# Kernel tuning notes

Hardware: AMD Instinct MI355X
Metric: run time of the kernel (lower is better)

## Reference

```python
import jax, jax.numpy as jnp
import numpy as np

EMBED_DIM = 1024
NUM_HEADS = 16
HEAD_DIM = EMBED_DIM // NUM_HEADS
B, S = 2, 2048


def setup_inputs() -> dict:
    key = jax.random.key(0)
    ks = jax.random.split(key, 9)
    d = EMBED_DIM
    scale = 1.0 / np.sqrt(d)
    inp = {
        "x": jax.random.normal(ks[0], (B, S, d), dtype=jnp.float32),
        "mask": jnp.ones((B, S), dtype=jnp.int32),
        "Wq": jax.random.normal(ks[1], (d, d), dtype=jnp.float32) * scale,
        "bq": jnp.zeros((d,), dtype=jnp.float32),
        "Wk": jax.random.normal(ks[2], (d, d), dtype=jnp.float32) * scale,
        "bk": jnp.zeros((d,), dtype=jnp.float32),
        "Wv": jax.random.normal(ks[3], (d, d), dtype=jnp.float32) * scale,
        "bv": jnp.zeros((d,), dtype=jnp.float32),
        "Wo": jax.random.normal(ks[4], (d, d), dtype=jnp.float32) * scale,
        "bo": jnp.zeros((d,), dtype=jnp.float32),
    }
    return inp


def reference(x, mask, Wq, bq, Wk, bk, Wv, bv, Wo, bo):
    b, s, _ = x.shape
    # projections; torch Linear computes x @ W.T + b
    q = (x @ Wq.T + bq).reshape(b, s, NUM_HEADS, HEAD_DIM).transpose(0, 2, 1, 3)
    k = (x @ Wk.T + bk).reshape(b, s, NUM_HEADS, HEAD_DIM).transpose(0, 2, 1, 3)
    v = (x @ Wv.T + bv).reshape(b, s, NUM_HEADS, HEAD_DIM).transpose(0, 2, 1, 3)
    scores = jnp.einsum("bhqd,bhkd->bhqk", q, k) / np.sqrt(HEAD_DIM)  # (B,H,S,S)
    m = (mask == 0)[:, None, None, :]  # broadcast over heads and query pos
    scores = jnp.where(m, jnp.float32(-1e9), scores)
    attn = jax.nn.softmax(scores, axis=-1)
    out = jnp.einsum("bhqk,bhkd->bhqd", attn, v)
    out = out.transpose(0, 2, 1, 3).reshape(b, s, EMBED_DIM)
    return out @ Wo.T + bo
```

## Files before the change

kernel.cpp:

```cpp
#include <hip/hip_runtime.h>

#define EMBED 1024
#define NHEAD 16
#define HDIM  64
#define BB    2
#define SS    2048

typedef __bf16 bf16x8 __attribute__((ext_vector_type(8)));
typedef float  f32x4  __attribute__((ext_vector_type(4)));
typedef _Float16 f16x4 __attribute__((ext_vector_type(4)));
typedef _Float16 f16x8 __attribute__((ext_vector_type(8)));
typedef __fp16 hf16x2 __attribute__((ext_vector_type(2)));

#if defined(__has_builtin)
#if __has_builtin(__builtin_amdgcn_exp2f)
#define EXP2(x) __builtin_amdgcn_exp2f(x)
#else
#define EXP2(x) exp2f(x)
#endif
#else
#define EXP2(x) exp2f(x)
#endif

__device__ __forceinline__ unsigned short f2bf(float f) {
  union { float f; unsigned u; } v; v.f = f;
  unsigned r = v.u + 0x7fffu + ((v.u >> 16) & 1u);
  return (unsigned short)(r >> 16);
}

__device__ __forceinline__ float bf2f(unsigned short u) {
  union { unsigned u; float f; } v; v.u = ((unsigned)u) << 16;
  return v.f;
}

__device__ __forceinline__ unsigned short f2h(float f) {
  union { _Float16 h; unsigned short u; } t;
  t.h = (_Float16)f;
  return t.u;
}

__device__ __forceinline__ void g2l16(const unsigned short* g, unsigned short* l) {
  __builtin_amdgcn_global_load_lds(
      (const __attribute__((address_space(1))) unsigned int*)g,
      (__attribute__((address_space(3))) unsigned int*)l, 16, 0, 0);
}

__global__ __launch_bounds__(256)
void cvt5_kernel(const float* __restrict__ x,  const float* __restrict__ Wq,
                 const float* __restrict__ Wk, const float* __restrict__ Wv,
                 const float* __restrict__ Wo, const int* __restrict__ mask,
                 unsigned short* __restrict__ xb,  unsigned short* __restrict__ Wqb,
                 unsigned short* __restrict__ Wkb, unsigned short* __restrict__ Wvb,
                 unsigned short* __restrict__ Wob, float* __restrict__ mbias) {
  const int i = blockIdx.x * 256 + threadIdx.x;
  if (i < (1 << 21)) {
    const float* src;
    unsigned short* dst;
    int j;
    if (i < (1 << 20)) {
      src = x; dst = xb; j = i;
    } else {
      const int t = i - (1 << 20);
      const int r = t >> 18;
      j = t & ((1 << 18) - 1);
      src = (r == 0) ? Wq : (r == 1) ? Wk : (r == 2) ? Wv : Wo;
      dst = (r == 0) ? Wqb : (r == 1) ? Wkb : (r == 2) ? Wvb : Wob;
    }
    const float4 f = ((const float4*)src)[j];
    ushort4 u;
    u.x = f2bf(f.x); u.y = f2bf(f.y); u.z = f2bf(f.z); u.w = f2bf(f.w);
    ((ushort4*)dst)[j] = u;
  } else {
    const int j = i - (1 << 21);
    const int4 m = ((const int4*)mask)[j];
    float4 o;
    o.x = m.x ? 0.f : -1e30f; o.y = m.y ? 0.f : -1e30f;
    o.z = m.z ? 0.f : -1e30f; o.w = m.w ? 0.f : -1e30f;
    ((float4*)mbias)[j] = o;
  }
}

template <typename EpiFn>
__device__ __forceinline__
void gemm_core(const unsigned short* __restrict__ A,
               const unsigned short* __restrict__ Bm,
               int m0, int n0, EpiFn epi) {
  __shared__ unsigned short sA[128 * 64];
  __shared__ unsigned short sB[128 * 64];
  const int tid = threadIdx.x;
  const int l  = tid & 63;
  const int w  = tid >> 6;
  const int lm = l & 15;
  const int qd = l >> 4;
  const int wm = w & 1;
  const int wn = w >> 1;

  f32x4 acc[4][4];
#pragma unroll
  for (int i = 0; i < 4; ++i)
#pragma unroll
    for (int j = 0; j < 4; ++j) acc[i][j] = (f32x4){0.f, 0.f, 0.f, 0.f};

  for (int k0 = 0; k0 < EMBED; k0 += 64) {
#pragma unroll
    for (int i = 0; i < 4; ++i) {
      const int t = i * 256 + tid;
      const int r = t >> 3;
      const int c = (t & 7) ^ (r & 7);
      g2l16(A + (m0 + r) * EMBED + k0 + c * 8, &sA[(i * 256 + (w << 6)) * 8]);
      g2l16(Bm + (n0 + r) * EMBED + k0 + c * 8, &sB[(i * 256 + (w << 6)) * 8]);
    }
    __syncthreads();
#pragma unroll
    for (int kk = 0; kk < 2; ++kk) {
      bf16x8 af[4], bfr[4];
#pragma unroll
      for (int mi = 0; mi < 4; ++mi) {
        const int R = wm * 64 + mi * 16 + lm;
        const int ch = R * 8 + (((kk << 2) + qd) ^ (R & 7));
        af[mi] = *(const bf16x8*)&sA[ch * 8];
      }
#pragma unroll
      for (int ni = 0; ni < 4; ++ni) {
        const int R = wn * 64 + ni * 16 + lm;
        const int ch = R * 8 + (((kk << 2) + qd) ^ (R & 7));
        bfr[ni] = *(const bf16x8*)&sB[ch * 8];
      }
#pragma unroll
      for (int mi = 0; mi < 4; ++mi)
#pragma unroll
        for (int ni = 0; ni < 4; ++ni)
          acc[mi][ni] = __builtin_amdgcn_mfma_f32_16x16x32_bf16(
              af[mi], bfr[ni], acc[mi][ni], 0, 0, 0);
    }
    __syncthreads();
  }

#pragma unroll
  for (int mi = 0; mi < 4; ++mi)
#pragma unroll
    for (int ni = 0; ni < 4; ++ni) {
      const int mb = m0 + wm * 64 + mi * 16 + qd * 4;
      const int n  = n0 + wn * 64 + ni * 16 + lm;
      epi(acc[mi][ni], mb, n);
    }
}

__device__ __forceinline__ void decode_tile(int flat, int& a0, int& b0) {
  const int sub = flat & 15;
  const int g = flat >> 4;
  a0 = ((g >> 2) * 2 + (sub >> 3));
  b0 = ((g & 3) * 8 + (sub & 7));
}

__global__ __launch_bounds__(256)
void gemm_qkv(const unsigned short* __restrict__ xb,
              const unsigned short* __restrict__ Wqb,
              const unsigned short* __restrict__ Wkb,
              const unsigned short* __restrict__ Wvb,
              const float* __restrict__ bq, const float* __restrict__ bk,
              const float* __restrict__ bv,
              unsigned short* __restrict__ Qb, unsigned short* __restrict__ Kb,
              unsigned short* __restrict__ VTb) {
  const int z = blockIdx.y;
  int a0, b0;
  decode_tile(blockIdx.x, a0, b0);
  if (z < 2) {
    const unsigned short* A = z ? Wkb : Wqb;
    const float* bias = z ? bk : bq;
    unsigned short* O = z ? Kb : Qb;
    const float scale = z ? 1.0f : 0.125f * 1.4426950408889634f;
    gemm_core(A, xb, a0 * 128, b0 * 128, [&](const f32x4& v, int mb, int n) {
      const float4 bvv = *(const float4*)&bias[mb];
      const int h = mb >> 6, d0 = mb & 63;
      const int b = n >> 11, s = n & 2047;
      ushort4 u;
      u.x = f2bf((v.x + bvv.x) * scale); u.y = f2bf((v.y + bvv.y) * scale);
      u.z = f2bf((v.z + bvv.z) * scale); u.w = f2bf((v.w + bvv.w) * scale);
      *(ushort4*)&O[(((b * NHEAD + h) * SS) + s) * HDIM + d0] = u;
    });
  } else {
    gemm_core(xb, Wvb, b0 * 128, a0 * 128, [&](const f32x4& v, int mb, int n) {
      const float bvv = bv[n];
      const int b = mb >> 11, s = mb & 2047;
      const int h = n >> 6, d = n & 63;
      const int col = (s & ~31) + ((s >> 2) & 3) * 8 + ((s >> 4) & 1) * 4;
      ushort4 u;
      u.x = f2h(v.x + bvv); u.y = f2h(v.y + bvv);
      u.z = f2h(v.z + bvv); u.w = f2h(v.w + bvv);
      *(ushort4*)&VTb[(((b * NHEAD + h) * HDIM) + d) * SS + col] = u;
    });
  }
}

__global__ __launch_bounds__(256)
void gemm_out(const unsigned short* __restrict__ Wob,
              const unsigned short* __restrict__ Ob,
              const float* __restrict__ bo, float* __restrict__ out) {
  int a0, b0;
  decode_tile(blockIdx.x, a0, b0);
  gemm_core(Wob, Ob, a0 * 128, b0 * 128, [&](const f32x4& v, int mb, int n) {
    const float4 bvv = *(const float4*)&bo[mb];
    float4 o;
    o.x = v.x + bvv.x; o.y = v.y + bvv.y; o.z = v.z + bvv.z; o.w = v.w + bvv.w;
    *(float4*)&out[n * EMBED + mb] = o;
  });
}

__global__ __launch_bounds__(256)
void attn_kernel(const unsigned short* __restrict__ Q,
                 const unsigned short* __restrict__ K,
                 const unsigned short* __restrict__ VT,
                 const float* __restrict__ mbias,
                 unsigned short* __restrict__ Op0,
                 unsigned short* __restrict__ Op1,
                 float* __restrict__ Lpart) {
  __shared__ unsigned short sK[2][64 * 64];
  __shared__ unsigned short sV[2][64 * 64];
  __shared__ float sM[1024];
  const int tid = threadIdx.x;
  const int l = tid & 63, w = tid >> 6;
  const int lm = l & 15, qd = l >> 4;
  const int b = blockIdx.z & 1, sp = blockIdx.z >> 1, h = blockIdx.y;
  const int q0 = blockIdx.x * 128 + w * 32;
  const unsigned short* Qh = Q + ((b * NHEAD + h) * SS) * HDIM;
  const unsigned short* Kh = K + ((b * NHEAD + h) * SS) * HDIM;
  const unsigned short* Vh = VT + ((b * NHEAD + h) * HDIM) * SS;
  const int k0 = sp * (SS / 2);
  unsigned short* Op = sp ? Op1 : Op0;
  float* Lp = Lpart + sp * (BB * NHEAD * SS);

  *(float4*)&sM[tid * 4] = *(const float4*)&mbias[b * SS + k0 + tid * 4];

  bf16x8 qf[2][2];
#pragma unroll
  for (int g = 0; g < 2; ++g) {
    qf[g][0] = *(const bf16x8*)&Qh[(q0 + g * 16 + lm) * HDIM + qd * 8];
    qf[g][1] = *(const bf16x8*)&Qh[(q0 + g * 16 + lm) * HDIM + 32 + qd * 8];
  }

  f32x4 Od[2][4];
#pragma unroll
  for (int g = 0; g < 2; ++g)
#pragma unroll
    for (int i = 0; i < 4; ++i) Od[g][i] = (f32x4){0.f, 0.f, 0.f, 0.f};
  float lsum[2] = {0.f, 0.f};

  auto stage = [&](int kb, int buf) {
#pragma unroll
    for (int i = 0; i < 2; ++i) {
      const int t = i * 256 + tid;
      const int r = t >> 3;
      const int c = (t & 7) ^ (r & 7);
      g2l16(Kh + (kb + r) * HDIM + c * 8, &sK[buf][(i * 256 + (w << 6)) * 8]);
      g2l16(Vh + r * SS + kb + c * 8, &sV[buf][(i * 256 + (w << 6)) * 8]);
    }
  };

  const int nIt = (SS / 2) / 64;
  stage(k0, 0);
  for (int it = 0; it < nIt; ++it) {
    __syncthreads();
    if (it + 1 < nIt) stage(k0 + (it + 1) * 64, (it + 1) & 1);
    const unsigned short* bK = sK[it & 1];
    const unsigned short* bV = sV[it & 1];
    const int mof = it * 64;

    f16x4 pf[2][4];
#pragma unroll
    for (int j = 0; j < 4; ++j) {
      const int R = j * 16 + lm;
      const bf16x8 k0f = *(const bf16x8*)&bK[(R * 8 + (qd ^ (lm & 7))) * 8];
      const bf16x8 k1f = *(const bf16x8*)&bK[(R * 8 + ((4 + qd) ^ (lm & 7))) * 8];
      const f32x4 binit = *(const f32x4*)&sM[mof + j * 16 + qd * 4];
#pragma unroll
      for (int g = 0; g < 2; ++g) {
        f32x4 t0 = binit;
        t0 = __builtin_amdgcn_mfma_f32_16x16x32_bf16(k0f, qf[g][0], t0, 0, 0, 0);
        t0 = __builtin_amdgcn_mfma_f32_16x16x32_bf16(k1f, qf[g][1], t0, 0, 0, 0);
        const float p0 = EXP2(t0[0]);
        const float p1 = EXP2(t0[1]);
        const float p2 = EXP2(t0[2]);
        const float p3 = EXP2(t0[3]);
        lsum[g] += (p0 + p1) + (p2 + p3);
        union { hf16x2 v[2]; f16x4 f; } pk;
        pk.v[0] = __builtin_amdgcn_cvt_pkrtz(p0, p1);
        pk.v[1] = __builtin_amdgcn_cvt_pkrtz(p2, p3);
        pf[g][j] = pk.f;
      }
    }

#pragma unroll
    for (int dt = 0; dt < 4; ++dt) {
      const int row = dt * 16 + lm;
#pragma unroll
      for (int p = 0; p < 2; ++p) {
        const int ch = (p * 4 + qd) ^ (lm & 7);
        const f16x8 v8 = *(const f16x8*)&bV[row * 64 + ch * 8];
        const f16x4 vlo = __builtin_shufflevector(v8, v8, 0, 1, 2, 3);
        const f16x4 vhi = __builtin_shufflevector(v8, v8, 4, 5, 6, 7);
#pragma unroll
        for (int g = 0; g < 2; ++g) {
          Od[g][dt] = __builtin_amdgcn_mfma_f32_16x16x16f16(vlo, pf[g][2 * p],
                                                            Od[g][dt], 0, 0, 0);
          Od[g][dt] = __builtin_amdgcn_mfma_f32_16x16x16f16(vhi, pf[g][2 * p + 1],
                                                            Od[g][dt], 0, 0, 0);
        }
      }
    }
  }

#pragma unroll
  for (int g = 0; g < 2; ++g) {
    float ls = lsum[g];
    ls += __shfl_xor(ls, 16);
    ls += __shfl_xor(ls, 32);
    if (qd == 0) Lp[(b * NHEAD + h) * SS + q0 + g * 16 + lm] = ls;
#pragma unroll
    for (int dt = 0; dt < 4; ++dt) {
      ushort4 u;
      u.x = f2bf(Od[g][dt][0]); u.y = f2bf(Od[g][dt][1]);
      u.z = f2bf(Od[g][dt][2]); u.w = f2bf(Od[g][dt][3]);
      *(ushort4*)&Op[(b * SS + q0 + g * 16 + lm) * EMBED + h * HDIM +
                     dt * 16 + qd * 4] = u;
    }
  }
}

__global__ __launch_bounds__(256)
void combine_kernel(unsigned short* __restrict__ Op0,
                    const unsigned short* __restrict__ Op1,
                    const float* __restrict__ Lpart) {
  const int i = blockIdx.x * 256 + threadIdx.x;
  const int base = i * 8;
  const int token = base >> 10;
  const int h = (base >> 6) & 15;
  const int b = token >> 11, q = token & 2047;
  const int lidx = (b * NHEAD + h) * SS + q;
  const int LN = BB * NHEAD * SS;
  const float ls = Lpart[lidx] + Lpart[LN + lidx];
  const float rinv = 1.f / ls;
#pragma unroll
  for (int k = 0; k < 2; ++k) {
    const ushort4 a = *(const ushort4*)&Op0[base + k * 4];
    const ushort4 c = *(const ushort4*)&Op1[base + k * 4];
    ushort4 o;
    o.x = f2bf((bf2f(a.x) + bf2f(c.x)) * rinv);
    o.y = f2bf((bf2f(a.y) + bf2f(c.y)) * rinv);
    o.z = f2bf((bf2f(a.z) + bf2f(c.z)) * rinv);
    o.w = f2bf((bf2f(a.w) + bf2f(c.w)) * rinv);
    *(ushort4*)&Op0[base + k * 4] = o;
  }
}

extern "C" void kernel_launch(void* const* d_in, const int* in_sizes, int n_in,
                              void* d_out, int out_size, void* d_ws, size_t ws_size,
                              hipStream_t stream) {
  const float* x  = (const float*)d_in[0];
  const int* mask = (const int*)d_in[1];
  const float* Wq = (const float*)d_in[2];
  const float* bq = (const float*)d_in[3];
  const float* Wk = (const float*)d_in[4];
  const float* bk = (const float*)d_in[5];
  const float* Wv = (const float*)d_in[6];
  const float* bv = (const float*)d_in[7];
  const float* Wo = (const float*)d_in[8];
  const float* bo = (const float*)d_in[9];
  float* out = (float*)d_out;

  char* ws = (char*)d_ws;
  const size_t MB = 1024 * 1024;
  unsigned short* xb  = (unsigned short*)(ws);
  unsigned short* Wqb = (unsigned short*)(ws + 8 * MB);
  unsigned short* Wkb = (unsigned short*)(ws + 10 * MB);
  unsigned short* Wvb = (unsigned short*)(ws + 12 * MB);
  unsigned short* Wob = (unsigned short*)(ws + 14 * MB);
  unsigned short* Qb  = (unsigned short*)(ws + 16 * MB);
  unsigned short* Kb  = (unsigned short*)(ws + 24 * MB);
  unsigned short* VTb = (unsigned short*)(ws + 32 * MB);
  float* mbb   = (float*)(ws + 40 * MB);
  float* Lpart = (float*)(ws + 40 * MB + 64 * 1024);
  unsigned short* Op0 = (unsigned short*)(ws + 41 * MB);
  unsigned short* Op1 = (unsigned short*)(ws + 49 * MB);

  cvt5_kernel<<<8196, 256, 0, stream>>>(x, Wq, Wk, Wv, Wo, mask,
                                        xb, Wqb, Wkb, Wvb, Wob, mbb);
  gemm_qkv<<<dim3(256, 3), 256, 0, stream>>>(xb, Wqb, Wkb, Wvb, bq, bk, bv,
                                             Qb, Kb, VTb);
  attn_kernel<<<dim3(16, 16, 4), 256, 0, stream>>>(Qb, Kb, VTb, mbb,
                                                   Op0, Op1, Lpart);
  combine_kernel<<<2048, 256, 0, stream>>>(Op0, Op1, Lpart);
  gemm_out<<<256, 256, 0, stream>>>(Wob, Op0, bo, out);
}
```

Before: 220.3 us.

## Rewrite attention PV path via LDS P-transpose and retile output GEMM

The attention kernel drops double-buffered K/V staging in favour of a single buffer with two barriers per iteration. It writes the probabilities P to a per-wave LDS scratch so the PV product can use the 16x16x32 f16 MFMA instead of pairs of 16x16x16. V^T is now stored in plain sequence order instead of the permuted column layout, and EXP2 always uses exp2f rather than the amdgcn builtin. gemm_out becomes a standalone 128x64-tile kernel with a 512-block grid and no load/compute overlap. Together these add LDS round trips and lose prefetch overlap in exchange for fewer MFMA instructions and more output-GEMM blocks.

Measured after the change: 239.4 us. 8.7% more time.

```diff
diff --git a/kernel.cpp b/kernel.cpp
--- a/kernel.cpp
+++ b/kernel.cpp
@@ -12,15 +12,7 @@
 typedef _Float16 f16x8 __attribute__((ext_vector_type(8)));
 typedef __fp16 hf16x2 __attribute__((ext_vector_type(2)));
 
-#if defined(__has_builtin)
-#if __has_builtin(__builtin_amdgcn_exp2f)
-#define EXP2(x) __builtin_amdgcn_exp2f(x)
-#else
 #define EXP2(x) exp2f(x)
-#endif
-#else
-#define EXP2(x) exp2f(x)
-#endif
 
 __device__ __forceinline__ unsigned short f2bf(float f) {
   union { float f; unsigned u; } v; v.f = f;
@@ -184,11 +176,10 @@
       const float bvv = bv[n];
       const int b = mb >> 11, s = mb & 2047;
       const int h = n >> 6, d = n & 63;
-      const int col = (s & ~31) + ((s >> 2) & 3) * 8 + ((s >> 4) & 1) * 4;
       ushort4 u;
       u.x = f2h(v.x + bvv); u.y = f2h(v.y + bvv);
       u.z = f2h(v.z + bvv); u.w = f2h(v.w + bvv);
-      *(ushort4*)&VTb[(((b * NHEAD + h) * HDIM) + d) * SS + col] = u;
+      *(ushort4*)&VTb[(((b * NHEAD + h) * HDIM) + d) * SS + s] = u;
     });
   }
 }
@@ -197,14 +188,77 @@
 void gemm_out(const unsigned short* __restrict__ Wob,
               const unsigned short* __restrict__ Ob,
               const float* __restrict__ bo, float* __restrict__ out) {
-  int a0, b0;
-  decode_tile(blockIdx.x, a0, b0);
-  gemm_core(Wob, Ob, a0 * 128, b0 * 128, [&](const f32x4& v, int mb, int n) {
-    const float4 bvv = *(const float4*)&bo[mb];
-    float4 o;
-    o.x = v.x + bvv.x; o.y = v.y + bvv.y; o.z = v.z + bvv.z; o.w = v.w + bvv.w;
-    *(float4*)&out[n * EMBED + mb] = o;
-  });
+  __shared__ unsigned short sA[128 * 64];
+  __shared__ unsigned short sB[64 * 64];
+  const int tid = threadIdx.x;
+  const int l  = tid & 63;
+  const int w  = tid >> 6;
+  const int lm = l & 15;
+  const int qd = l >> 4;
+  const int wm = w & 1;
+  const int wn = w >> 1;
+  const int m0 = blockIdx.y * 128;
+  const int n0 = blockIdx.x * 64;
+
+  f32x4 acc[4][2];
+#pragma unroll
+  for (int i = 0; i < 4; ++i)
+#pragma unroll
+    for (int j = 0; j < 2; ++j) acc[i][j] = (f32x4){0.f, 0.f, 0.f, 0.f};
+
+  for (int k0 = 0; k0 < EMBED; k0 += 64) {
+#pragma unroll
+    for (int i = 0; i < 4; ++i) {
+      const int t = i * 256 + tid;
+      const int r = t >> 3;
+      const int c = (t & 7) ^ (r & 7);
+      g2l16(Wob + (m0 + r) * EMBED + k0 + c * 8, &sA[(i * 256 + (w << 6)) * 8]);
+    }
+#pragma unroll
+    for (int i = 0; i < 2; ++i) {
+      const int t = i * 256 + tid;
+      const int r = t >> 3;
+      const int c = (t & 7) ^ (r & 7);
+      g2l16(Ob + (n0 + r) * EMBED + k0 + c * 8, &sB[(i * 256 + (w << 6)) * 8]);
+    }
+    __syncthreads();
+#pragma unroll
+    for (int kk = 0; kk < 2; ++kk) {
+      bf16x8 af[4], bfr[2];
+#pragma unroll
+      for (int mi = 0; mi < 4; ++mi) {
+        const int R = wm * 64 + mi * 16 + lm;
+        const int ch = R * 8 + (((kk << 2) + qd) ^ (R & 7));
+        af[mi] = *(const bf16x8*)&sA[ch * 8];
+      }
+#pragma unroll
+      for (int ni = 0; ni < 2; ++ni) {
+        const int R = wn * 32 + ni * 16 + lm;
+        const int ch = R * 8 + (((kk << 2) + qd) ^ (R & 7));
+        bfr[ni] = *(const bf16x8*)&sB[ch * 8];
+      }
+#pragma unroll
+      for (int mi = 0; mi < 4; ++mi)
+#pragma unroll
+        for (int ni = 0; ni < 2; ++ni)
+          acc[mi][ni] = __builtin_amdgcn_mfma_f32_16x16x32_bf16(
+              af[mi], bfr[ni], acc[mi][ni], 0, 0, 0);
+    }
+    __syncthreads();
+  }
+
+#pragma unroll
+  for (int mi = 0; mi < 4; ++mi)
+#pragma unroll
+    for (int ni = 0; ni < 2; ++ni) {
+      const int mb = m0 + wm * 64 + mi * 16 + qd * 4;
+      const int n  = n0 + wn * 32 + ni * 16 + lm;
+      const float4 bvv = *(const float4*)&bo[mb];
+      const f32x4 v = acc[mi][ni];
+      float4 o;
+      o.x = v.x + bvv.x; o.y = v.y + bvv.y; o.z = v.z + bvv.z; o.w = v.w + bvv.w;
+      *(float4*)&out[n * EMBED + mb] = o;
+    }
 }
 
 __global__ __launch_bounds__(256)
@@ -215,8 +269,9 @@
                  unsigned short* __restrict__ Op0,
                  unsigned short* __restrict__ Op1,
                  float* __restrict__ Lpart) {
-  __shared__ unsigned short sK[2][64 * 64];
-  __shared__ unsigned short sV[2][64 * 64];
+  __shared__ unsigned short sK[64 * 64];
+  __shared__ unsigned short sV[64 * 64];
+  __shared__ unsigned short sP[4][16 * 68];
   __shared__ float sM[1024];
   const int tid = threadIdx.x;
   const int l = tid & 63, w = tid >> 6;
@@ -229,6 +284,7 @@
   const int k0 = sp * (SS / 2);
   unsigned short* Op = sp ? Op1 : Op0;
   float* Lp = Lpart + sp * (BB * NHEAD * SS);
+  unsigned short* Pw = sP[w];
 
   *(float4*)&sM[tid * 4] = *(const float4*)&mbias[b * SS + k0 + tid * 4];
 
@@ -246,36 +302,38 @@
     for (int i = 0; i < 4; ++i) Od[g][i] = (f32x4){0.f, 0.f, 0.f, 0.f};
   float lsum[2] = {0.f, 0.f};
 
-  auto stage = [&](int kb, int buf) {
+  for (int it = 0; it < 16; ++it) {
+    const int kb = k0 + it * 64;
 #pragma unroll
     for (int i = 0; i < 2; ++i) {
       const int t = i * 256 + tid;
       const int r = t >> 3;
       const int c = (t & 7) ^ (r & 7);
-      g2l16(Kh + (kb + r) * HDIM + c * 8, &sK[buf][(i * 256 + (w << 6)) * 8]);
-      g2l16(Vh + r * SS + kb + c * 8, &sV[buf][(i * 256 + (w << 6)) * 8]);
-    }
-  };
-
-  const int nIt = (SS / 2) / 64;
-  stage(k0, 0);
-  for (int it = 0; it < nIt; ++it) {
-    __syncthreads();
-    if (it + 1 < nIt) stage(k0 + (it + 1) * 64, (it + 1) & 1);
-    const unsigned short* bK = sK[it & 1];
-    const unsigned short* bV = sV[it & 1];
-    const int mof = it * 64;
-
-    f16x4 pf[2][4];
-#pragma unroll
-    for (int j = 0; j < 4; ++j) {
-      const int R = j * 16 + lm;
-      const bf16x8 k0f = *(const bf16x8*)&bK[(R * 8 + (qd ^ (lm & 7))) * 8];
-      const bf16x8 k1f = *(const bf16x8*)&bK[(R * 8 + ((4 + qd) ^ (lm & 7))) * 8];
-      const f32x4 binit = *(const f32x4*)&sM[mof + j * 16 + qd * 4];
-#pragma unroll
-      for (int g = 0; g < 2; ++g) {
-        f32x4 t0 = binit;
+      g2l16(Kh + (kb + r) * HDIM + c * 8, &sK[(i * 256 + (w << 6)) * 8]);
+      g2l16(Vh + r * SS + kb + c * 8, &sV[(i * 256 + (w << 6)) * 8]);
+    }
+    __syncthreads();
+
+    f16x8 vf[4][2];
+#pragma unroll
+    for (int dt = 0; dt < 4; ++dt) {
+      const int row = dt * 16 + lm;
+#pragma unroll
+      for (int kp = 0; kp < 2; ++kp) {
+        const int ch = (kp * 4 + qd) ^ (lm & 7);
+        vf[dt][kp] = *(const f16x8*)&sV[row * 64 + ch * 8];
+      }
+    }
+
+#pragma unroll
+    for (int g = 0; g < 2; ++g) {
+      f16x4 pf[4];
+#pragma unroll
+      for (int j = 0; j < 4; ++j) {
+        const int R = j * 16 + lm;
+        const bf16x8 k0f = *(const bf16x8*)&sK[(R * 8 + (qd ^ (lm & 7))) * 8];
+        const bf16x8 k1f = *(const bf16x8*)&sK[(R * 8 + ((4 + qd) ^ (lm & 7))) * 8];
+        f32x4 t0 = *(const f32x4*)&sM[it * 64 + j * 16 + qd * 4];
         t0 = __builtin_amdgcn_mfma_f32_16x16x32_bf16(k0f, qf[g][0], t0, 0, 0, 0);
         t0 = __builtin_amdgcn_mfma_f32_16x16x32_bf16(k1f, qf[g][1], t0, 0, 0, 0);
         const float p0 = EXP2(t0[0]);
@@ -286,28 +344,21 @@
         union { hf16x2 v[2]; f16x4 f; } pk;
         pk.v[0] = __builtin_amdgcn_cvt_pkrtz(p0, p1);
         pk.v[1] = __builtin_amdgcn_cvt_pkrtz(p2, p3);
-        pf[g][j] = pk.f;
-      }
-    }
-
-#pragma unroll
-    for (int dt = 0; dt < 4; ++dt) {
-      const int row = dt * 16 + lm;
-#pragma unroll
-      for (int p = 0; p < 2; ++p) {
-        const int ch = (p * 4 + qd) ^ (lm & 7);
-        const f16x8 v8 = *(const f16x8*)&bV[row * 64 + ch * 8];
-        const f16x4 vlo = __builtin_shufflevector(v8, v8, 0, 1, 2, 3);
-        const f16x4 vhi = __builtin_shufflevector(v8, v8, 4, 5, 6, 7);
-#pragma unroll
-        for (int g = 0; g < 2; ++g) {
-          Od[g][dt] = __builtin_amdgcn_mfma_f32_16x16x16f16(vlo, pf[g][2 * p],
-                                                            Od[g][dt], 0, 0, 0);
-          Od[g][dt] = __builtin_amdgcn_mfma_f32_16x16x16f16(vhi, pf[g][2 * p + 1],
-                                                            Od[g][dt], 0, 0, 0);
-        }
-      }
-    }
+        pf[j] = pk.f;
+      }
+#pragma unroll
+      for (int j = 0; j < 4; ++j)
+        *(f16x4*)&Pw[lm * 68 + j * 16 + qd * 4] = pf[j];
+#pragma unroll
+      for (int kp = 0; kp < 2; ++kp) {
+        const f16x8 pb = *(const f16x8*)&Pw[lm * 68 + kp * 32 + qd * 8];
+#pragma unroll
+        for (int dt = 0; dt < 4; ++dt)
+          Od[g][dt] = __builtin_amdgcn_mfma_f32_16x16x32_f16(vf[dt][kp], pb,
+                                                             Od[g][dt], 0, 0, 0);
+      }
+    }
+    __syncthreads();
   }
 
 #pragma unroll
@@ -390,5 +441,5 @@
   attn_kernel<<<dim3(16, 16, 4), 256, 0, stream>>>(Qb, Kb, VTb, mbb,
                                                    Op0, Op1, Lpart);
   combine_kernel<<<2048, 256, 0, stream>>>(Op0, Op1, Lpart);
-  gemm_out<<<256, 256, 0, stream>>>(Wob, Op0, bo, out);
-}
+  gemm_out<<<dim3(64, 8), 256, 0, stream>>>(Wob, Op0, bo, out);
+}
```
